# Kernel optimization log

Measured on AMD Instinct MI355X. Metric: run time of the kernel, lower is better.

## Reference

```python
import jax, jax.numpy as jnp
import numpy as np

NC = 151  # number of object classes (VG)
NR = 51   # number of relation classes (VG)


def setup_inputs() -> dict:
    key = jax.random.key(0)
    ks = jax.random.split(key, 10)
    B, N, D = 32, 100, 4096
    H = D // 4
    w = lambda k, shape, fan_in: (jax.random.normal(k, shape, jnp.float32) / np.sqrt(fan_in).astype(np.float32))
    return {
        "encoder_reps": jax.random.normal(ks[0], (B * N, D), jnp.float32),
        "W_comp": w(ks[1], (D, H), D),        # obj_comp Linear (no bias)
        "W_ou1": w(ks[2], (H, H), H),         # ou1 Linear
        "W_ofc": w(ks[3], (H, H), H),         # ofc_u Linear
        "W_decomp": w(ks[4], (H, D), H),      # obj_decomp Linear
        "conv1": w(ks[5], (10, NR, 3, 3), NR * 9),  # Conv2d(51,10,3,pad=1)
        "conv2": w(ks[6], (5, 10, 3, 3), 10 * 9),   # Conv2d(10,5,3,pad=1)
        "conv3": w(ks[7], (1, 5, 1, 1), 5),         # Conv2d(5,1,1)
        "freq_emb": jax.random.normal(ks[8], (NC * NC, NR), jnp.float32) * 0.01,
        "obj_preds": jax.random.randint(ks[9], (B * N,), 0, NC),
        "num_obj": 100,
    }


def reference(encoder_reps, W_comp, W_ou1, W_ofc, W_decomp, conv1, conv2, conv3, freq_emb, obj_preds, num_obj):
    T, D = encoder_reps.shape
    N = num_obj
    B = T // N
    relu = jax.nn.relu
    # obj_comp then per-image ou1 (vectorized over images)
    comp = relu(encoder_reps @ W_comp).reshape(B, N, -1)   # [B,N,H]
    obj_u1 = relu(comp @ W_ou1)                             # [B,N,H]
    # product-index frequency-bias gather: emb[subj*NC + obj]
    labels = obj_preds.reshape(B, N)
    pair_idx = labels[:, :, None] * NC + labels[:, None, :]  # [B,N,N]
    adj_fg = freq_emb[pair_idx]                               # [B,N,N,NR]
    # adjacency net: Conv-Conv-Conv-Tanh over the NxN 'image' with NR channels
    x = jnp.transpose(adj_fg, (0, 3, 1, 2))                   # [B,NR,N,N]
    dn = ("NCHW", "OIHW", "NCHW")
    x = jax.lax.conv_general_dilated(x, conv1, (1, 1), "SAME", dimension_numbers=dn)
    x = jax.lax.conv_general_dilated(x, conv2, (1, 1), "SAME", dimension_numbers=dn)
    x = jnp.tanh(jax.lax.conv_general_dilated(x, conv3, (1, 1), "SAME", dimension_numbers=dn))
    adj = x[:, 0]                                             # [B,N,N]
    # graph message passing: adj @ obj_u1, then ofc_u / decomp + residual
    ofl_u = jnp.einsum("bnm,bmh->bnh", adj, obj_u1).reshape(T, -1)
    u_m = relu(ofl_u @ W_ofc)
    decomp = relu(u_m @ W_decomp)
    return decomp + encoder_reps
```

## Files before the change

### kernel.cpp

```cpp
#include <hip/hip_runtime.h>
#include <cmath>

#define NCC 151
#define NRCH 51
#define BDIM 32
#define NOBJ 100
#define DDIM 4096
#define HDIM 1024
#define TDIM (BDIM * NOBJ)

typedef __bf16 bf16_t;
typedef __bf16 bf16x8 __attribute__((ext_vector_type(8)));
typedef __bf16 bf16x4 __attribute__((ext_vector_type(4)));
typedef float f32x4 __attribute__((ext_vector_type(4)));

template <bool RELU, bool ADDBF16, int SPLITK, int MODE>
__global__ __launch_bounds__(256) void gemm_bf16(
    const bf16_t* __restrict__ A,
    const bf16_t* __restrict__ Bt,
    const bf16_t* __restrict__ add,
    void* __restrict__ Cout,
    int N, int K, size_t MN) {
  __shared__ __align__(16) bf16_t Asm[2][128 * 64];
  __shared__ __align__(16) bf16_t Bsm[2][128 * 64];
  const int tid = threadIdx.x;
  const int lane = tid & 63;
  const int w = tid >> 6;
  const int wm = w >> 1, wn = w & 1;

  const int nx = gridDim.x, ny = gridDim.y, nz = gridDim.z;
  const int h = blockIdx.x + nx * (blockIdx.y + ny * blockIdx.z);
  int bx, by, bz;
  if (MODE == 3) {
    const int xcd = h & 7, s = h >> 3;
    bz = xcd >> 1;
    const int half = xcd & 1;
    if (half == 1 && s >= 96) return;
    const int c = s / 40;
    if (c < 2) {
      const int within = s % 40;
      bx = within / 5;
      by = (half ? 13 : 0) + c * 5 + within % 5;
    } else if (half == 0) {
      const int w2 = s - 80;
      bx = w2 / 3;
      by = 10 + w2 % 3;
    } else {
      const int w2 = s - 80;
      bx = w2 / 2;
      by = 23 + w2 % 2;
    }
  } else {
    const int nwg = nx * ny * nz;
    const int q = nwg >> 3;
    const int lin = (h & 7) * q + (h >> 3);
    by = lin % ny;
    const int r = lin / ny;
    bx = r % nx;
    bz = r / nx;
  }

  const int bm = by * 128, bn = bx * 128;
  const int lr = lane & 15;
  const int lk = lane >> 4;

  int kBeg = 0, kEnd = K;
  if (SPLITK > 1) {
    const int chunk = (((K / 64) + SPLITK - 1) / SPLITK) * 64;
    kBeg = bz * chunk;
    kEnd = min(K, kBeg + chunk);
  }

  f32x4 acc[4][4];
#pragma unroll
  for (int m = 0; m < 4; ++m)
#pragma unroll
    for (int n = 0; n < 4; ++n) acc[m][n] = (f32x4){0.f, 0.f, 0.f, 0.f};

  const int srow = tid >> 3;
  const int sslot = tid & 7;

  auto stage = [&](int buf, int kt) {
#pragma unroll
    for (int i = 0; i < 4; ++i) {
      const int row = i * 32 + srow;
      const int kc = sslot ^ (row & 7);
      const bf16_t* ga = A + (size_t)(bm + row) * K + kt + kc * 8;
      const bf16_t* gb = Bt + (size_t)(bn + row) * K + kt + kc * 8;
      __builtin_amdgcn_global_load_lds(
          (const __attribute__((address_space(1))) void*)ga,
          (__attribute__((address_space(3))) void*)((char*)&Asm[buf][0] +
                                                    i * 4096 + w * 1024),
          16, 0, 0);
      __builtin_amdgcn_global_load_lds(
          (const __attribute__((address_space(1))) void*)gb,
          (__attribute__((address_space(3))) void*)((char*)&Bsm[buf][0] +
                                                    i * 4096 + w * 1024),
          16, 0, 0);
    }
  };

  stage(0, kBeg);
  __syncthreads();

  int cur = 0;
  for (int kt = kBeg; kt < kEnd; kt += 64) {
    const bool more = (kt + 64 < kEnd);
    if (more) stage(cur ^ 1, kt + 64);

    char* ldsA = (char*)&Asm[cur][0];
    char* ldsB = (char*)&Bsm[cur][0];
    bf16x8 af[4][2], bfr[4][2];
#pragma unroll
    for (int m = 0; m < 4; ++m) {
      const int row = wm * 64 + m * 16 + lr;
#pragma unroll
      for (int kk = 0; kk < 2; ++kk) {
        const int slot = kk * 4 + lk;
        af[m][kk] =
            *(const bf16x8*)(ldsA + row * 128 + ((slot ^ (lr & 7)) << 4));
      }
    }
#pragma unroll
    for (int n = 0; n < 4; ++n) {
      const int row = wn * 64 + n * 16 + lr;
#pragma unroll
      for (int kk = 0; kk < 2; ++kk) {
        const int slot = kk * 4 + lk;
        bfr[n][kk] =
            *(const bf16x8*)(ldsB + row * 128 + ((slot ^ (lr & 7)) << 4));
      }
    }
#pragma unroll
    for (int m = 0; m < 4; ++m)
#pragma unroll
      for (int n = 0; n < 4; ++n) {
        acc[m][n] = __builtin_amdgcn_mfma_f32_16x16x32_bf16(
            af[m][0], bfr[n][0], acc[m][n], 0, 0, 0);
        acc[m][n] = __builtin_amdgcn_mfma_f32_16x16x32_bf16(
            af[m][1], bfr[n][1], acc[m][n], 0, 0, 0);
      }

    if (more) __syncthreads();
    cur ^= 1;
  }

  const int or0 = bm + wm * 64 + lk * 4;
  const int oc0 = bn + wn * 64 + lr;
#pragma unroll
  for (int m = 0; m < 4; ++m)
#pragma unroll
    for (int n = 0; n < 4; ++n)
#pragma unroll
      for (int r = 0; r < 4; ++r) {
        float v = acc[m][n][r];
        const size_t off = (size_t)(or0 + m * 16 + r) * N + (oc0 + n * 16);
        if (SPLITK > 1) {
          ((bf16_t*)Cout)[bz * MN + off] = (bf16_t)v;
        } else {
          if (RELU) v = fmaxf(v, 0.f);
          if (ADDBF16)
            ((float*)Cout)[off] = v + (float)add[off];
          else
            ((bf16_t*)Cout)[off] = (bf16_t)v;
        }
      }
}

template <int NPART>
__global__ __launch_bounds__(256) void reduceN_kernel(
    const bf16_t* __restrict__ p, bf16_t* __restrict__ out, int n8,
    size_t MN) {
  int i = blockIdx.x * 256 + threadIdx.x;
  if (i >= n8) return;
  float s[8] = {};
#pragma unroll
  for (int z = 0; z < NPART; ++z) {
    bf16x8 v = *(const bf16x8*)(p + z * MN + (size_t)i * 8);
#pragma unroll
    for (int j = 0; j < 8; ++j) s[j] += (float)v[j];
  }
  bf16x8 o;
#pragma unroll
  for (int j = 0; j < 8; ++j) o[j] = (bf16_t)fmaxf(s[j], 0.f);
  *(bf16x8*)(out + (size_t)i * 8) = o;
}

__global__ __launch_bounds__(256) void cvt_bf16_kernel(
    const float* __restrict__ in, bf16_t* __restrict__ out, int n4) {
  int i = blockIdx.x * 256 + threadIdx.x;
  if (i >= n4) return;
  float4 v = ((const float4*)in)[i];
  bf16x4 o = {(bf16_t)v.x, (bf16_t)v.y, (bf16_t)v.z, (bf16_t)v.w};
  ((bf16x4*)out)[i] = o;
}

__global__ __launch_bounds__(256) void transT_kernel(
    const float* __restrict__ in, bf16_t* __restrict__ out, int K, int N) {
  __shared__ float t[32][33];
  const int n0 = blockIdx.x * 32, k0 = blockIdx.y * 32;
  const int tx = threadIdx.x & 31, ty = threadIdx.x >> 5;
#pragma unroll
  for (int i = 0; i < 4; ++i)
    t[ty + i * 8][tx] = in[(size_t)(k0 + ty + i * 8) * N + n0 + tx];
  __syncthreads();
#pragma unroll
  for (int i = 0; i < 4; ++i)
    out[(size_t)(n0 + ty + i * 8) * K + k0 + tx] = (bf16_t)t[tx][ty + i * 8];
}

__global__ __launch_bounds__(256) void prep_w1r_kernel(
    const float* __restrict__ w1, float* __restrict__ w1r) {
  int idx = blockIdx.x * 256 + threadIdx.x;
  if (idx >= NRCH * 90) return;
  int ci = idx / 90, r = idx % 90, k9 = r / 10, co = r % 10;
  w1r[idx] = w1[((co * NRCH + ci) * 3 + k9 / 3) * 3 + (k9 % 3)];
}

__global__ __launch_bounds__(128) void femb1_kernel(
    const float* __restrict__ femb, const float* __restrict__ w1r,
    float* __restrict__ femb1) {
  __shared__ float row[NRCH];
  const int p = blockIdx.x;
  if (threadIdx.x < NRCH)
    row[threadIdx.x] = femb[(size_t)p * NRCH + threadIdx.x];
  __syncthreads();
  const int t = threadIdx.x;
  if (t >= 90) return;
  float acc = 0.f;
#pragma unroll
  for (int ci = 0; ci < NRCH; ++ci) acc += row[ci] * w1r[ci * 90 + t];
  femb1[((size_t)p * 9 + t / 10) * 12 + (t % 10)] = acc;
}

__global__ __launch_bounds__(256) void conv1g_kernel(
    const int* __restrict__ preds, const float* __restrict__ femb1,
    float* __restrict__ x1) {
  int idx = blockIdx.x * 256 + threadIdx.x;
  if (idx >= BDIM * NOBJ * NOBJ) return;
  int j = idx % NOBJ;
  int i = (idx / NOBJ) % NOBJ;
  int b = idx / (NOBJ * NOBJ);
  const int* pr = preds + b * NOBJ;
  int li[3], lj[3];
#pragma unroll
  for (int d = 0; d < 3; ++d) {
    li[d] = pr[min(max(i + d - 1, 0), NOBJ - 1)];
    lj[d] = pr[min(max(j + d - 1, 0), NOBJ - 1)];
  }
  f32x4 a0 = {0.f, 0.f, 0.f, 0.f}, a1 = a0, a2 = a0;
#pragma unroll
  for (int kh = 0; kh < 3; ++kh) {
    int ii = i + kh - 1;
    if (ii < 0 || ii >= NOBJ) continue;
#pragma unroll
    for (int kw = 0; kw < 3; ++kw) {
      int jj = j + kw - 1;
      if (jj < 0 || jj >= NOBJ) continue;
      int p = li[kh] * NCC + lj[kw];
      const f32x4* f =
          (const f32x4*)(femb1 + ((size_t)p * 9 + kh * 3 + kw) * 12);
      a0 += f[0];
      a1 += f[1];
      a2 += f[2];
    }
  }
  f32x4* o = (f32x4*)(x1 + (size_t)idx * 12);
  o[0] = a0;
  o[1] = a1;
  o[2] = a2;
}

__global__ __launch_bounds__(256) void conv23_kernel(
    const float* __restrict__ x1, const float* __restrict__ w2,
    const float* __restrict__ w3, float* __restrict__ adj) {
  __shared__ float w[90];
  if (threadIdx.x < 90) {
    const int k9 = threadIdx.x / 10, c2 = threadIdx.x % 10;
    float a = 0.f;
#pragma unroll
    for (int c3 = 0; c3 < 5; ++c3)
      a += w3[c3] * w2[(c3 * 10 + c2) * 9 + k9];
    w[threadIdx.x] = a;
  }
  __syncthreads();
  int idx = blockIdx.x * 256 + threadIdx.x;
  if (idx >= BDIM * NOBJ * NOBJ) return;
  int j = idx % NOBJ;
  int i = (idx / NOBJ) % NOBJ;
  int b = idx / (NOBJ * NOBJ);
  float acc = 0.f;
  const float* xb = x1 + (size_t)b * NOBJ * NOBJ * 12;
#pragma unroll
  for (int kh = 0; kh < 3; ++kh) {
    int ii = i + kh - 1;
    if (ii < 0 || ii >= NOBJ) continue;
#pragma unroll
    for (int kw = 0; kw < 3; ++kw) {
      int jj = j + kw - 1;
      if (jj < 0 || jj >= NOBJ) continue;
      const float* xr = xb + (ii * NOBJ + jj) * 12;
      const float* wr = w + (kh * 3 + kw) * 10;
#pragma unroll
      for (int c = 0; c < 10; ++c) acc += wr[c] * xr[c];
    }
  }
  adj[idx] = tanhf(acc);
}

__global__ __launch_bounds__(256) void einsum_mfma_kernel(
    const float* __restrict__ adj,
    const bf16_t* __restrict__ u1,
    bf16_t* __restrict__ ofl) {
  __shared__ __align__(16) bf16_t As[128 * 128];
  __shared__ __align__(16) bf16_t Us[128 * 128];
  const int b = blockIdx.y;
  const int h0 = blockIdx.x * 128;
  const int tid = threadIdx.x, lane = tid & 63, w = tid >> 6;
  const int wm = w >> 1, wn = w & 1;
  const int lr = lane & 15, lk = lane >> 4;

  {
    f32x4 z = {0.f, 0.f, 0.f, 0.f};
#pragma unroll
    for (int i = 0; i < 8; ++i) ((f32x4*)As)[tid + i * 256] = z;
#pragma unroll
    for (int i = 0; i < 8; ++i) ((f32x4*)Us)[tid + i * 256] = z;
  }
  __syncthreads();

  const float* ab = adj + (size_t)b * 10000;
#pragma unroll
  for (int i = 0; i < 10; ++i) {
    int idx = tid + i * 256;
    if (idx < 2500) {
      int row = idx / 25, kc = idx % 25;
      f32x4 v = ((const f32x4*)ab)[idx];
      bf16x4 o = {(bf16_t)v[0], (bf16_t)v[1], (bf16_t)v[2], (bf16_t)v[3]};
      int slot = kc >> 1;
      *(bf16x4*)((char*)As + row * 256 + ((slot ^ (row & 7)) << 4) +
                 (kc & 1) * 8) = o;
    }
  }

  const bf16_t* ub = u1 + (size_t)b * 100 * HDIM + h0;
#pragma unroll
  for (int i = 0; i < 7; ++i) {
    int idx = tid + i * 256;
    if (idx < 1600) {
      int hc = idx / 100, m = idx % 100;
      bf16x8 v = *(const bf16x8*)(ub + (size_t)m * HDIM + hc * 8);
      int slot = m >> 3, mr = m & 7;
#pragma unroll
      for (int j = 0; j < 8; ++j) {
        int h = hc * 8 + j;
        *((bf16_t*)((char*)Us + h * 256 + ((slot ^ (h & 7)) << 4) + mr * 2)) =
            v[j];
      }
    }
  }
  __syncthreads();

  f32x4 acc[4][4];
#pragma unroll
  for (int m = 0; m < 4; ++m)
#pragma unroll
    for (int n = 0; n < 4; ++n) acc[m][n] = (f32x4){0.f, 0.f, 0.f, 0.f};

#pragma unroll
  for (int ks = 0; ks < 4; ++ks) {
    bf16x8 a[4], u[4];
#pragma unroll
    for (int m = 0; m < 4; ++m) {
      int row = wm * 64 + m * 16 + lr;
      int slot = ks * 4 + lk;
      a[m] = *(const bf16x8*)((char*)As + row * 256 + ((slot ^ (lr & 7)) << 4));
    }
#pragma unroll
    for (int n = 0; n < 4; ++n) {
      int row = wn * 64 + n * 16 + lr;
      int slot = ks * 4 + lk;
      u[n] = *(const bf16x8*)((char*)Us + row * 256 + ((slot ^ (lr & 7)) << 4));
    }
#pragma unroll
    for (int m = 0; m < 4; ++m)
#pragma unroll
      for (int n = 0; n < 4; ++n)
        acc[m][n] = __builtin_amdgcn_mfma_f32_16x16x32_bf16(a[m], u[n],
                                                            acc[m][n], 0, 0, 0);
  }

  const int or0 = wm * 64 + lk * 4;
  const int oc0 = h0 + wn * 64 + lr;
#pragma unroll
  for (int m = 0; m < 4; ++m)
#pragma unroll
    for (int n = 0; n < 4; ++n)
#pragma unroll
      for (int r = 0; r < 4; ++r) {
        int row = or0 + m * 16 + r;
        if (row < 100)
          ofl[((size_t)b * 100 + row) * HDIM + oc0 + n * 16] =
              (bf16_t)acc[m][n][r];
      }
}

extern "C" void kernel_launch(void* const* d_in, const int* in_sizes, int n_in,
                              void* d_out, int out_size, void* d_ws,
                              size_t ws_size, hipStream_t stream) {
  const float* enc = (const float*)d_in[0];
  const float* W_comp = (const float*)d_in[1];
  const float* W_ou1 = (const float*)d_in[2];
  const float* W_ofc = (const float*)d_in[3];
  const float* W_dec = (const float*)d_in[4];
  const float* conv1w = (const float*)d_in[5];
  const float* conv2w = (const float*)d_in[6];
  const float* conv3w = (const float*)d_in[7];
  const float* femb = (const float*)d_in[8];
  const int* preds = (const int*)d_in[9];
  float* out = (float*)d_out;
  char* wsb = (char*)d_ws;

  const size_t MN = (size_t)TDIM * HDIM;

  bf16_t* encb   = (bf16_t*)(wsb + 0);
  bf16_t* WcompT = (bf16_t*)(wsb + 26214400);
  bf16_t* comp   = (bf16_t*)(wsb + 34603008);
  bf16_t* part4  = (bf16_t*)(wsb + 41156608);
  bf16_t* Wou1T  = (bf16_t*)(wsb + 41156608);
  float*  femb1  = (float*)(wsb + 43272512);
  float*  w1r    = (float*)(wsb + 53122560);
  float*  x1     = (float*)(wsb + 54402560);
  bf16_t* obj_u1 = (bf16_t*)(wsb + 69762560);
  float*  adj    = (float*)(wsb + 76316160);
  bf16_t* ofl_u  = (bf16_t*)(wsb + 26214400);
  bf16_t* WofcT  = (bf16_t*)(wsb + 32768000);
  bf16_t* u_m    = (bf16_t*)(wsb + 34865152);
  bf16_t* WdecT  = (bf16_t*)(wsb + 41418752);

  const int n8 = (int)(MN / 8);

  cvt_bf16_kernel<<<(TDIM * DDIM / 4 + 255) / 256, 256, 0, stream>>>(
      enc, encb, TDIM * DDIM / 4);
  transT_kernel<<<dim3(HDIM / 32, DDIM / 32), 256, 0, stream>>>(
      W_comp, WcompT, DDIM, HDIM);

  gemm_bf16<false, false, 4, 3><<<dim3(832, 1, 1), 256, 0, stream>>>(
      encb, WcompT, nullptr, part4, HDIM, DDIM, MN);
  reduceN_kernel<4><<<n8 / 256, 256, 0, stream>>>(part4, comp, n8, MN);

  transT_kernel<<<dim3(HDIM / 32, HDIM / 32), 256, 0, stream>>>(
      W_ou1, Wou1T, HDIM, HDIM);
  gemm_bf16<true, false, 1, 0>
      <<<dim3(HDIM / 128, TDIM / 128), 256, 0, stream>>>(
          comp, Wou1T, nullptr, obj_u1, HDIM, HDIM, MN);

  prep_w1r_kernel<<<(NRCH * 90 + 255) / 256, 256, 0, stream>>>(conv1w, w1r);
  femb1_kernel<<<NCC * NCC, 128, 0, stream>>>(femb, w1r, femb1);
  conv1g_kernel<<<(BDIM * NOBJ * NOBJ + 255) / 256, 256, 0, stream>>>(
      preds, femb1, x1);
  conv23_kernel<<<(BDIM * NOBJ * NOBJ + 255) / 256, 256, 0, stream>>>(
      x1, conv2w, conv3w, adj);

  transT_kernel<<<dim3(HDIM / 32, HDIM / 32), 256, 0, stream>>>(
      W_ofc, WofcT, HDIM, HDIM);
  transT_kernel<<<dim3(DDIM / 32, HDIM / 32), 256, 0, stream>>>(
      W_dec, WdecT, HDIM, DDIM);

  einsum_mfma_kernel<<<dim3(HDIM / 128, BDIM), 256, 0, stream>>>(adj, obj_u1,
                                                                 ofl_u);

  gemm_bf16<true, false, 1, 0>
      <<<dim3(HDIM / 128, TDIM / 128), 256, 0, stream>>>(
          ofl_u, WofcT, nullptr, u_m, HDIM, HDIM, MN);

  gemm_bf16<true, true, 1, 0>
      <<<dim3(DDIM / 128, TDIM / 128), 256, 0, stream>>>(
          u_m, WdecT, encb, out, DDIM, HDIM, MN);
}
```

Before: 251.0 us.

## Fuse prep kernels, fuse conv stages with LDS tiling, single-buffer GEMM LDS

Merges the bf16 conversion, all weight transposes and the conv1 weight reorder into one prep kernel to cut launches. Fuses the conv1 gather and conv2/conv3 stages into one tiled kernel that keeps the 18x18 halo of conv1 outputs in shared memory instead of writing and re-reading x1 from global memory. It also changes the GEMM from double-buffered to single-buffered LDS with two barriers per k-step. That reduces LDS use, which may raise occupancy, but it loses the overlap between loads and MFMA work.

```diff
diff --git a/kernel.cpp b/kernel.cpp
--- a/kernel.cpp
+++ b/kernel.cpp
@@ -21,8 +21,8 @@
     const bf16_t* __restrict__ add,
     void* __restrict__ Cout,
     int N, int K, size_t MN) {
-  __shared__ __align__(16) bf16_t Asm[2][128 * 64];
-  __shared__ __align__(16) bf16_t Bsm[2][128 * 64];
+  __shared__ __align__(16) bf16_t Asm[128 * 64];
+  __shared__ __align__(16) bf16_t Bsm[128 * 64];
   const int tid = threadIdx.x;
   const int lane = tid & 63;
   const int w = tid >> 6;
@@ -61,8 +61,7 @@
   }
 
   const int bm = by * 128, bn = bx * 128;
-  const int lr = lane & 15;
-  const int lk = lane >> 4;
+  const int lr = lane & 15, lk = lane >> 4;
 
   int kBeg = 0, kEnd = K;
   if (SPLITK > 1) {
@@ -77,10 +76,12 @@
 #pragma unroll
     for (int n = 0; n < 4; ++n) acc[m][n] = (f32x4){0.f, 0.f, 0.f, 0.f};
 
-  const int srow = tid >> 3;
-  const int sslot = tid & 7;
-
-  auto stage = [&](int buf, int kt) {
+  const int srow = tid >> 3, sslot = tid & 7;
+  char* ldsA = (char*)Asm;
+  char* ldsB = (char*)Bsm;
+
+  for (int kt = kBeg; kt < kEnd; kt += 64) {
+    __syncthreads();
 #pragma unroll
     for (int i = 0; i < 4; ++i) {
       const int row = i * 32 + srow;
@@ -89,27 +90,15 @@
       const bf16_t* gb = Bt + (size_t)(bn + row) * K + kt + kc * 8;
       __builtin_amdgcn_global_load_lds(
           (const __attribute__((address_space(1))) void*)ga,
-          (__attribute__((address_space(3))) void*)((char*)&Asm[buf][0] +
-                                                    i * 4096 + w * 1024),
+          (__attribute__((address_space(3))) void*)(ldsA + i * 4096 + w * 1024),
           16, 0, 0);
       __builtin_amdgcn_global_load_lds(
           (const __attribute__((address_space(1))) void*)gb,
-          (__attribute__((address_space(3))) void*)((char*)&Bsm[buf][0] +
-                                                    i * 4096 + w * 1024),
+          (__attribute__((address_space(3))) void*)(ldsB + i * 4096 + w * 1024),
           16, 0, 0);
     }
-  };
-
-  stage(0, kBeg);
-  __syncthreads();
-
-  int cur = 0;
-  for (int kt = kBeg; kt < kEnd; kt += 64) {
-    const bool more = (kt + 64 < kEnd);
-    if (more) stage(cur ^ 1, kt + 64);
-
-    char* ldsA = (char*)&Asm[cur][0];
-    char* ldsB = (char*)&Bsm[cur][0];
+    __syncthreads();
+
     bf16x8 af[4][2], bfr[4][2];
 #pragma unroll
     for (int m = 0; m < 4; ++m) {
@@ -140,9 +129,6 @@
         acc[m][n] = __builtin_amdgcn_mfma_f32_16x16x32_bf16(
             af[m][1], bfr[n][1], acc[m][n], 0, 0, 0);
       }
-
-    if (more) __syncthreads();
-    cur ^= 1;
   }
 
   const int or0 = bm + wm * 64 + lk * 4;
@@ -186,20 +172,52 @@
   *(bf16x8*)(out + (size_t)i * 8) = o;
 }
 
-__global__ __launch_bounds__(256) void cvt_bf16_kernel(
-    const float* __restrict__ in, bf16_t* __restrict__ out, int n4) {
-  int i = blockIdx.x * 256 + threadIdx.x;
-  if (i >= n4) return;
-  float4 v = ((const float4*)in)[i];
-  bf16x4 o = {(bf16_t)v.x, (bf16_t)v.y, (bf16_t)v.z, (bf16_t)v.w};
-  ((bf16x4*)out)[i] = o;
-}
-
-__global__ __launch_bounds__(256) void transT_kernel(
-    const float* __restrict__ in, bf16_t* __restrict__ out, int K, int N) {
+__global__ __launch_bounds__(256) void prep_all(
+    const float* __restrict__ enc, const float* __restrict__ Wcomp,
+    const float* __restrict__ Wou1, const float* __restrict__ Wofc,
+    const float* __restrict__ Wdec, const float* __restrict__ w1,
+    bf16_t* __restrict__ encb, bf16_t* __restrict__ WcompT,
+    bf16_t* __restrict__ Wou1T, bf16_t* __restrict__ WofcT,
+    bf16_t* __restrict__ WdecT, float* __restrict__ w1r) {
   __shared__ float t[32][33];
-  const int n0 = blockIdx.x * 32, k0 = blockIdx.y * 32;
-  const int tx = threadIdx.x & 31, ty = threadIdx.x >> 5;
+  const int tid = threadIdx.x;
+  int blk = blockIdx.x;
+
+  if (blk < 12800) {
+    const int i = blk * 256 + tid;
+    float4 v = ((const float4*)enc)[i];
+    bf16x4 o = {(bf16_t)v.x, (bf16_t)v.y, (bf16_t)v.z, (bf16_t)v.w};
+    ((bf16x4*)encb)[i] = o;
+    return;
+  }
+  blk -= 12800;
+
+  const float* in;
+  bf16_t* out;
+  int K, N, nx;
+  if (blk < 4096) {
+    in = Wcomp; out = WcompT; K = 4096; N = 1024; nx = 32;
+  } else if (blk < 4096 + 1024) {
+    blk -= 4096;
+    in = Wou1; out = Wou1T; K = 1024; N = 1024; nx = 32;
+  } else if (blk < 4096 + 2048) {
+    blk -= 4096 + 1024;
+    in = Wofc; out = WofcT; K = 1024; N = 1024; nx = 32;
+  } else if (blk < 4096 + 2048 + 4096) {
+    blk -= 4096 + 2048;
+    in = Wdec; out = WdecT; K = 1024; N = 4096; nx = 128;
+  } else {
+    blk -= 4096 + 2048 + 4096;
+    const int idx = blk * 256 + tid;
+    if (idx < NRCH * 90) {
+      int ci = idx / 90, r = idx % 90, k9 = r / 10, co = r % 10;
+      w1r[idx] = w1[((co * NRCH + ci) * 3 + k9 / 3) * 3 + (k9 % 3)];
+    }
+    return;
+  }
+
+  const int n0 = (blk % nx) * 32, k0 = (blk / nx) * 32;
+  const int tx = tid & 31, ty = tid >> 5;
 #pragma unroll
   for (int i = 0; i < 4; ++i)
     t[ty + i * 8][tx] = in[(size_t)(k0 + ty + i * 8) * N + n0 + tx];
@@ -207,14 +225,6 @@
 #pragma unroll
   for (int i = 0; i < 4; ++i)
     out[(size_t)(n0 + ty + i * 8) * K + k0 + tx] = (bf16_t)t[tx][ty + i * 8];
-}
-
-__global__ __launch_bounds__(256) void prep_w1r_kernel(
-    const float* __restrict__ w1, float* __restrict__ w1r) {
-  int idx = blockIdx.x * 256 + threadIdx.x;
-  if (idx >= NRCH * 90) return;
-  int ci = idx / 90, r = idx % 90, k9 = r / 10, co = r % 10;
-  w1r[idx] = w1[((co * NRCH + ci) * 3 + k9 / 3) * 3 + (k9 % 3)];
 }
 
 __global__ __launch_bounds__(128) void femb1_kernel(
@@ -233,84 +243,75 @@
   femb1[((size_t)p * 9 + t / 10) * 12 + (t % 10)] = acc;
 }
 
-__global__ __launch_bounds__(256) void conv1g_kernel(
+__global__ __launch_bounds__(256) void conv_fused(
     const int* __restrict__ preds, const float* __restrict__ femb1,
-    float* __restrict__ x1) {
-  int idx = blockIdx.x * 256 + threadIdx.x;
-  if (idx >= BDIM * NOBJ * NOBJ) return;
-  int j = idx % NOBJ;
-  int i = (idx / NOBJ) % NOBJ;
-  int b = idx / (NOBJ * NOBJ);
-  const int* pr = preds + b * NOBJ;
-  int li[3], lj[3];
-#pragma unroll
-  for (int d = 0; d < 3; ++d) {
-    li[d] = pr[min(max(i + d - 1, 0), NOBJ - 1)];
-    lj[d] = pr[min(max(j + d - 1, 0), NOBJ - 1)];
-  }
-  f32x4 a0 = {0.f, 0.f, 0.f, 0.f}, a1 = a0, a2 = a0;
-#pragma unroll
-  for (int kh = 0; kh < 3; ++kh) {
-    int ii = i + kh - 1;
-    if (ii < 0 || ii >= NOBJ) continue;
-#pragma unroll
-    for (int kw = 0; kw < 3; ++kw) {
-      int jj = j + kw - 1;
-      if (jj < 0 || jj >= NOBJ) continue;
-      int p = li[kh] * NCC + lj[kw];
-      const f32x4* f =
-          (const f32x4*)(femb1 + ((size_t)p * 9 + kh * 3 + kw) * 12);
-      a0 += f[0];
-      a1 += f[1];
-      a2 += f[2];
-    }
-  }
-  f32x4* o = (f32x4*)(x1 + (size_t)idx * 12);
-  o[0] = a0;
-  o[1] = a1;
-  o[2] = a2;
-}
-
-__global__ __launch_bounds__(256) void conv23_kernel(
-    const float* __restrict__ x1, const float* __restrict__ w2,
-    const float* __restrict__ w3, float* __restrict__ adj) {
+    const float* __restrict__ w2, const float* __restrict__ w3,
+    float* __restrict__ adj) {
+  __shared__ float xt[18][18][12];
   __shared__ float w[90];
-  if (threadIdx.x < 90) {
-    const int k9 = threadIdx.x / 10, c2 = threadIdx.x % 10;
+  const int tid = threadIdx.x;
+  const int b = blockIdx.z;
+  const int ti = blockIdx.y * 16, tj = blockIdx.x * 16;
+
+  if (tid < 90) {
+    const int k9 = tid / 10, c2 = tid % 10;
     float a = 0.f;
 #pragma unroll
     for (int c3 = 0; c3 < 5; ++c3)
       a += w3[c3] * w2[(c3 * 10 + c2) * 9 + k9];
-    w[threadIdx.x] = a;
+    w[tid] = a;
+  }
+
+  const int* pr = preds + b * NOBJ;
+
+  for (int t = tid; t < 324; t += 256) {
+    const int hi = t / 18, wj = t % 18;
+    const int ii = ti - 1 + hi, jj = tj - 1 + wj;
+    f32x4 a0 = {0.f, 0.f, 0.f, 0.f}, a1 = a0, a2 = a0;
+    if (ii >= 0 && ii < NOBJ && jj >= 0 && jj < NOBJ) {
+#pragma unroll
+      for (int kh = 0; kh < 3; ++kh) {
+        const int i2 = ii + kh - 1;
+        if (i2 < 0 || i2 >= NOBJ) continue;
+        const int li = pr[i2];
+#pragma unroll
+        for (int kw = 0; kw < 3; ++kw) {
+          const int j2 = jj + kw - 1;
+          if (j2 < 0 || j2 >= NOBJ) continue;
+          const int p = li * NCC + pr[j2];
+          const f32x4* f =
+              (const f32x4*)(femb1 + ((size_t)p * 9 + kh * 3 + kw) * 12);
+          a0 += f[0];
+          a1 += f[1];
+          a2 += f[2];
+        }
+      }
+    }
+    f32x4* o = (f32x4*)&xt[hi][wj][0];
+    o[0] = a0;
+    o[1] = a1;
+    o[2] = a2;
   }
   __syncthreads();
-  int idx = blockIdx.x * 256 + threadIdx.x;
-  if (idx >= BDIM * NOBJ * NOBJ) return;
-  int j = idx % NOBJ;
-  int i = (idx / NOBJ) % NOBJ;
-  int b = idx / (NOBJ * NOBJ);
+
+  const int di = tid >> 4, dj = tid & 15;
+  const int i = ti + di, j = tj + dj;
+  if (i >= NOBJ || j >= NOBJ) return;
   float acc = 0.f;
-  const float* xb = x1 + (size_t)b * NOBJ * NOBJ * 12;
-#pragma unroll
-  for (int kh = 0; kh < 3; ++kh) {
-    int ii = i + kh - 1;
-    if (ii < 0 || ii >= NOBJ) continue;
+#pragma unroll
+  for (int kh = 0; kh < 3; ++kh)
 #pragma unroll
     for (int kw = 0; kw < 3; ++kw) {
-      int jj = j + kw - 1;
-      if (jj < 0 || jj >= NOBJ) continue;
-      const float* xr = xb + (ii * NOBJ + jj) * 12;
+      const float* xr = &xt[di + kh][dj + kw][0];
       const float* wr = w + (kh * 3 + kw) * 10;
 #pragma unroll
       for (int c = 0; c < 10; ++c) acc += wr[c] * xr[c];
     }
-  }
-  adj[idx] = tanhf(acc);
+  adj[((size_t)b * NOBJ + i) * NOBJ + j] = tanhf(acc);
 }
 
 __global__ __launch_bounds__(256) void einsum_mfma_kernel(
-    const float* __restrict__ adj,
-    const bf16_t* __restrict__ u1,
+    const float* __restrict__ adj, const bf16_t* __restrict__ u1,
     bf16_t* __restrict__ ofl) {
   __shared__ __align__(16) bf16_t As[128 * 128];
   __shared__ __align__(16) bf16_t Us[128 * 128];
@@ -425,47 +426,35 @@
 
   bf16_t* encb   = (bf16_t*)(wsb + 0);
   bf16_t* WcompT = (bf16_t*)(wsb + 26214400);
-  bf16_t* comp   = (bf16_t*)(wsb + 34603008);
-  bf16_t* part4  = (bf16_t*)(wsb + 41156608);
-  bf16_t* Wou1T  = (bf16_t*)(wsb + 41156608);
-  float*  femb1  = (float*)(wsb + 43272512);
-  float*  w1r    = (float*)(wsb + 53122560);
-  float*  x1     = (float*)(wsb + 54402560);
-  bf16_t* obj_u1 = (bf16_t*)(wsb + 69762560);
-  float*  adj    = (float*)(wsb + 76316160);
-  bf16_t* ofl_u  = (bf16_t*)(wsb + 26214400);
-  bf16_t* WofcT  = (bf16_t*)(wsb + 32768000);
-  bf16_t* u_m    = (bf16_t*)(wsb + 34865152);
-  bf16_t* WdecT  = (bf16_t*)(wsb + 41418752);
+  bf16_t* Wou1T  = (bf16_t*)(wsb + 34603008);
+  bf16_t* WofcT  = (bf16_t*)(wsb + 36700160);
+  bf16_t* WdecT  = (bf16_t*)(wsb + 38797312);
+  float*  w1r    = (float*)(wsb + 47185920);
+  bf16_t* comp   = (bf16_t*)(wsb + 47204352);
+  bf16_t* part4  = (bf16_t*)(wsb + 53757952);
+  float*  femb1  = (float*)(wsb + 53757952);
+  bf16_t* obj_u1 = (bf16_t*)(wsb + 63608064);
+  float*  adj    = (float*)(wsb + 70161664);
+  bf16_t* u_m    = (bf16_t*)(wsb + 71441664);
+  bf16_t* ofl_u  = (bf16_t*)(wsb + 47204352);
 
   const int n8 = (int)(MN / 8);
 
-  cvt_bf16_kernel<<<(TDIM * DDIM / 4 + 255) / 256, 256, 0, stream>>>(
-      enc, encb, TDIM * DDIM / 4);
-  transT_kernel<<<dim3(HDIM / 32, DDIM / 32), 256, 0, stream>>>(
-      W_comp, WcompT, DDIM, HDIM);
+  prep_all<<<23058, 256, 0, stream>>>(enc, W_comp, W_ou1, W_ofc, W_dec,
+                                      conv1w, encb, WcompT, Wou1T, WofcT,
+                                      WdecT, w1r);
 
   gemm_bf16<false, false, 4, 3><<<dim3(832, 1, 1), 256, 0, stream>>>(
       encb, WcompT, nullptr, part4, HDIM, DDIM, MN);
   reduceN_kernel<4><<<n8 / 256, 256, 0, stream>>>(part4, comp, n8, MN);
 
-  transT_kernel<<<dim3(HDIM / 32, HDIM / 32), 256, 0, stream>>>(
-      W_ou1, Wou1T, HDIM, HDIM);
   gemm_bf16<true, false, 1, 0>
       <<<dim3(HDIM / 128, TDIM / 128), 256, 0, stream>>>(
           comp, Wou1T, nullptr, obj_u1, HDIM, HDIM, MN);
 
-  prep_w1r_kernel<<<(NRCH * 90 + 255) / 256, 256, 0, stream>>>(conv1w, w1r);
   femb1_kernel<<<NCC * NCC, 128, 0, stream>>>(femb, w1r, femb1);
-  conv1g_kernel<<<(BDIM * NOBJ * NOBJ + 255) / 256, 256, 0, stream>>>(
-      preds, femb1, x1);
-  conv23_kernel<<<(BDIM * NOBJ * NOBJ + 255) / 256, 256, 0, stream>>>(
-      x1, conv2w, conv3w, adj);
-
-  transT_kernel<<<dim3(HDIM / 32, HDIM / 32), 256, 0, stream>>>(
-      W_ofc, WofcT, HDIM, HDIM);
-  transT_kernel<<<dim3(DDIM / 32, HDIM / 32), 256, 0, stream>>>(
-      W_dec, WdecT, HDIM, DDIM);
+  conv_fused<<<dim3(7, 7, BDIM), 256, 0, stream>>>(preds, femb1, conv2w,
+                                                   conv3w, adj);
 
   einsum_mfma_kernel<<<dim3(HDIM / 128, BDIM), 256, 0, stream>>>(adj, obj_u1,
                                                                  ofl_u);
```

After: 243.2 us. 1.03x faster.
